# Optimization experiments

Hardware: AMD Instinct MI355X
Metric: run time of the kernel (lower is better)

## Reference

```python
import jax, jax.numpy as jnp
import numpy as np

N, C, A, CI = 32768, 512, 64, 1024  # n_locations, content_size, address_size, controller_input_size
EPS = 1e-7


def setup_inputs() -> dict:
    key = jax.random.key(0)
    ks = jax.random.split(key, 12)
    g = lambda i, shape, s=1.0: jax.random.normal(ks[i], shape, dtype=jnp.float32) * s
    xav = lambda i, shape: g(i, shape, float(np.sqrt(2.0 / (shape[0] + shape[1]))))
    return {
        "controller_hidden_state": g(0, (N, 1)),
        "controller_input": g(1, (CI, 1)),
        "memory_contents": g(2, (N, C), 0.5),
        "memory_addresses": xav(3, (N, A)),
        "exp_mov_avg_similarity": g(4, (N, 1), 0.1),
        "W_query": xav(5, (C + A, N)),
        "b_query": jnp.zeros((C + A, 1), jnp.float32),
        "u_sharpen": xav(6, (1, N)),
        "b_sharpen": jnp.zeros((1,), jnp.float32),
        "u_lru": xav(7, (1, N)),
        "b_lru": jnp.zeros((1,), jnp.float32),
        "W_erase": xav(8, (C, N)),
        "b_erase": jnp.zeros((C, 1), jnp.float32),
        "W_content_hidden": xav(9, (C, N)),
        "W_content_input": xav(10, (C, CI)),
        "u_content_alpha": xav(11, (N + CI, 1)),
        "b_content_alpha": jnp.zeros((1, 1), jnp.float32),
    }


def reference(controller_hidden_state, controller_input, memory_contents, memory_addresses,
              exp_mov_avg_similarity, W_query, b_query, u_sharpen, b_sharpen, u_lru, b_lru,
              W_erase, b_erase, W_content_hidden, W_content_input, u_content_alpha,
              b_content_alpha):
    h, x = controller_hidden_state, controller_input
    # ---- address_memory ----
    full_mem = jnp.concatenate([memory_addresses, memory_contents], axis=1)  # [N, A+C]
    query = W_query @ h + b_query                                            # [A+C, 1]
    beta = jax.nn.softplus(u_sharpen @ h + b_sharpen) + 1.0                  # [1, 1]
    q = query[:, 0]
    q_norm = jnp.maximum(jnp.linalg.norm(q), EPS)
    m_norm = jnp.maximum(jnp.linalg.norm(full_mem, axis=1), EPS)             # [N]
    cos = (full_mem @ q) / (m_norm * q_norm)                                 # [N] cosine sim per location
    sim = (beta[0, 0] * cos)[:, None]                                        # [N, 1]
    gamma = jax.nn.sigmoid(u_lru @ h + b_lru)                                # [1, 1] LRU gate
    addr = jax.nn.softmax(sim - gamma * exp_mov_avg_similarity, axis=0)      # [N, 1]
    # (state buffer update, next-step only): new_ema = 0.1*ema + 0.9*sim
    # ---- update (vectorized erase/write over all N locations) ----
    erase = W_erase @ h + b_erase                                            # [C, 1]
    alpha = u_content_alpha.T @ jnp.concatenate([h, x], axis=0) + b_content_alpha  # [1, 1]
    cand = jax.nn.relu(W_content_hidden @ h + alpha * (W_content_input @ x))       # [C, 1]
    new_mem = (1.0 - addr * erase.T) * memory_contents + addr * cand.T       # [N, C]
    # ---- read (on updated memory) ----
    new_full = jnp.concatenate([memory_addresses, new_mem], axis=1)          # [N, A+C]
    read = new_full.T @ addr                                                 # [A+C, 1]
    return read
```

## Files before the change

### kernel.cpp

```cpp
#include <hip/hip_runtime.h>
#include <hip/hip_bf16.h>
#include <math.h>

#define NN 32768
#define CC 512
#define AA 64
#define CIN 1024
#define EPSV 1e-7f


#define QOFF 2128
#define STOFF 2704
#define SCOFF 4240
#define PAOFF 5264
#define PMOFF 38032

typedef float floatx4 __attribute__((ext_vector_type(4)));

__device__ __forceinline__ float4 ntload4(const float4* p) {
    floatx4 v = __builtin_nontemporal_load(reinterpret_cast<const floatx4*>(p));
    return make_float4(v.x, v.y, v.z, v.w);
}
__device__ __forceinline__ float ntloadf(const float* p) {
    return __builtin_nontemporal_load(p);
}

__global__ __launch_bounds__(256) void k1_gemv(
    const float* __restrict__ h, const float* __restrict__ x,
    const float* __restrict__ Wq, const float* __restrict__ Wer,
    const float* __restrict__ Wch, const float* __restrict__ Wci,
    const float* __restrict__ ush, const float* __restrict__ ulr,
    const float* __restrict__ uca, float* __restrict__ ws)
{
    const int b = blockIdx.x, tid = threadIdx.x;
    const int wave = tid >> 6, lane = tid & 63;
    __shared__ float hs[4096];
    __shared__ float red[4][8];

    if (b < 1600) {
        const int rg = b >> 3, chunk = b & 7;
        const float4* h4 = reinterpret_cast<const float4*>(h) + chunk * 1024;
        float4* hs4 = reinterpret_cast<float4*>(hs);
        #pragma unroll
        for (int k = 0; k < 4; ++k) hs4[k * 256 + tid] = h4[k * 256 + tid];
        __syncthreads();
        const int r0 = rg * 8;
        const float* mat; int base;
        if (r0 < 576)       { mat = Wq;  base = 0; }
        else if (r0 < 1088) { mat = Wer; base = 576; }
        else                { mat = Wch; base = 1088; }
        const float4* m4 = reinterpret_cast<const float4*>(
            mat + (size_t)(r0 - base) * NN + chunk * 4096);
        const int rs = NN / 4;
        float acc[8] = {0,0,0,0,0,0,0,0};
        float4 cur[8];
        #pragma unroll
        for (int r = 0; r < 8; ++r) cur[r] = ntload4(m4 + (size_t)r * rs + tid);
        #pragma unroll
        for (int it = 0; it < 4; ++it) {
            float4 nxt[8];
            if (it < 3) {
                #pragma unroll
                for (int r = 0; r < 8; ++r)
                    nxt[r] = ntload4(m4 + (size_t)r * rs + (it + 1) * 256 + tid);
            }
            float4 hb = hs4[it * 256 + tid];
            #pragma unroll
            for (int r = 0; r < 8; ++r)
                acc[r] += cur[r].x * hb.x + cur[r].y * hb.y +
                          cur[r].z * hb.z + cur[r].w * hb.w;
            if (it < 3) {
                #pragma unroll
                for (int r = 0; r < 8; ++r) cur[r] = nxt[r];
            }
        }
        #pragma unroll
        for (int r = 0; r < 8; ++r) {
            #pragma unroll
            for (int off = 32; off >= 1; off >>= 1)
                acc[r] += __shfl_xor(acc[r], off);
        }
        if (lane == 0) {
            #pragma unroll
            for (int r = 0; r < 8; ++r) red[wave][r] = acc[r];
        }
        __syncthreads();
        if (tid < 8) {
            float v = red[0][tid] + red[1][tid] + red[2][tid] + red[3][tid];
            atomicAdd(ws + r0 + tid, v);
        }
    } else if (b < 1664) {
        const int rg = b - 1600;
        float4 xv = reinterpret_cast<const float4*>(x)[tid];
        const float4* m4 = reinterpret_cast<const float4*>(
            Wci + (size_t)rg * 8 * CIN);
        float acc[8];
        #pragma unroll
        for (int r = 0; r < 8; ++r) {
            float4 a = ntload4(m4 + r * 256 + tid);
            acc[r] = a.x * xv.x + a.y * xv.y + a.z * xv.z + a.w * xv.w;
        }
        #pragma unroll
        for (int r = 0; r < 8; ++r) {
            #pragma unroll
            for (int off = 32; off >= 1; off >>= 1)
                acc[r] += __shfl_xor(acc[r], off);
        }
        if (lane == 0) {
            #pragma unroll
            for (int r = 0; r < 8; ++r) red[wave][r] = acc[r];
        }
        __syncthreads();
        if (tid < 8) {
            float v = red[0][tid] + red[1][tid] + red[2][tid] + red[3][tid];
            ws[1600 + rg * 8 + tid] = v;
        }
    } else {
        const int t = b - 1664, sd = t >> 3, chunk = t & 7;
        const float* vec = (sd == 0) ? ush : (sd == 1) ? ulr : uca;
        const float4* v4 = reinterpret_cast<const float4*>(vec) + chunk * 1024;
        const float4* h4 = reinterpret_cast<const float4*>(h) + chunk * 1024;
        float acc = 0.f;
        #pragma unroll
        for (int it = 0; it < 4; ++it) {
            float4 a = v4[it * 256 + tid];
            float4 hb = h4[it * 256 + tid];
            acc += a.x * hb.x + a.y * hb.y + a.z * hb.z + a.w * hb.w;
        }
        if (sd == 2 && chunk == 0) {
            float4 a = reinterpret_cast<const float4*>(uca)[NN / 4 + tid];
            float4 xv = reinterpret_cast<const float4*>(x)[tid];
            acc += a.x * xv.x + a.y * xv.y + a.z * xv.z + a.w * xv.w;
        }
        #pragma unroll
        for (int off = 32; off >= 1; off >>= 1)
            acc += __shfl_xor(acc, off);
        if (lane == 0) red[wave][0] = acc;
        __syncthreads();
        if (tid == 0)
            atomicAdd(ws + 2112 + sd,
                      red[0][0] + red[1][0] + red[2][0] + red[3][0]);
    }
}

__global__ __launch_bounds__(256) void k1b_scalars(
    const float* __restrict__ bq, const float* __restrict__ bsh,
    const float* __restrict__ blr, const float* __restrict__ bca,
    float* __restrict__ ws)
{
    __shared__ float red[256];
    const int tid = threadIdx.x;
    float s = 0.f;
    for (int j = tid; j < 576; j += 256) {
        float q = ws[j] + bq[j];
        ws[QOFF + j] = q;
        s += q * q;
    }
    red[tid] = s; __syncthreads();
    for (int st = 128; st > 0; st >>= 1) {
        if (tid < st) red[tid] += red[tid + st];
        __syncthreads();
    }
    if (tid == 0) {
        float qn = fmaxf(sqrtf(red[0]), EPSV);
        float bp = ws[2112] + bsh[0];
        float beta = (bp > 20.f ? bp : log1pf(expf(bp))) + 1.0f;
        float gp = ws[2113] + blr[0];
        float gamma = 1.f / (1.f + expf(-gp));
        float alpha = ws[2114] + bca[0];
        ws[2112] = beta; ws[2113] = gamma; ws[2114] = alpha; ws[2115] = qn;
    }
}

__global__ __launch_bounds__(512) void k2f_fused(
    const float* __restrict__ Mm, const float* __restrict__ Ad,
    const float* __restrict__ ema, const float* __restrict__ ws,
    float* __restrict__ pm, float* __restrict__ pa, float* __restrict__ stats)
{
    __shared__ float lw[8][1092];
    const int b = blockIdx.x, tid = threadIdx.x, wave = tid >> 6, lane = tid & 63;
    const float beta = ws[2112], gamma = ws[2113], qn = ws[2115];
    const float ql = ws[QOFF + lane];
    float4 qa = *reinterpret_cast<const float4*>(ws + QOFF + 64 + lane * 8);
    float4 qb = *reinterpret_cast<const float4*>(ws + QOFF + 68 + lane * 8);
    float qm[8] = {qa.x, qa.y, qa.z, qa.w, qb.x, qb.y, qb.z, qb.w};

    float a1[8] = {0,0,0,0,0,0,0,0};
    float a2[8] = {0,0,0,0,0,0,0,0};
    float aA = 0.f, m_run = -1e30f, Z = 0.f, S2 = 0.f;
    const int base = b * 64 + wave * 8;
    for (int j = 0; j < 8; ++j) {
        const int i = base + j;
        float a = ntloadf(Ad + (size_t)i * AA + lane);
        float4 m0 = ntload4(reinterpret_cast<const float4*>(Mm + (size_t)i * CC + lane * 8));
        float4 m1 = ntload4(reinterpret_cast<const float4*>(Mm + (size_t)i * CC + lane * 8 + 4));
        float mm[8] = {m0.x, m0.y, m0.z, m0.w, m1.x, m1.y, m1.z, m1.w};
        float dot = a * ql, nn = a * a;
        #pragma unroll
        for (int k = 0; k < 8; ++k) { float f = mm[k]; dot += f * qm[k]; nn += f * f; }
        #pragma unroll
        for (int off = 32; off >= 1; off >>= 1) {
            dot += __shfl_xor(dot, off);
            nn  += __shfl_xor(nn, off);
        }
        float mn = fmaxf(sqrtf(nn), EPSV);
        float s = beta * (dot / (mn * qn)) - gamma * ema[i];
        if (s > m_run) {
            float f = expf(m_run - s);
            float f2 = f * f;
            Z *= f; S2 *= f2; aA *= f;
            #pragma unroll
            for (int k = 0; k < 8; ++k) { a1[k] *= f; a2[k] *= f2; }
            m_run = s;
        }
        float w = expf(s - m_run);
        float w2 = w * w;
        Z += w; S2 += w2; aA += w * a;
        #pragma unroll
        for (int k = 0; k < 8; ++k) { a1[k] += w * mm[k]; a2[k] += w2 * mm[k]; }
    }
    #pragma unroll
    for (int k = 0; k < 8; ++k) {
        lw[wave][lane * 8 + k] = a1[k];
        lw[wave][512 + lane * 8 + k] = a2[k];
    }
    lw[wave][1024 + lane] = aA;
    if (lane == 0) { lw[wave][1088] = m_run; lw[wave][1089] = Z; lw[wave][1090] = S2; }
    __syncthreads();
    float mb = lw[0][1088];
    #pragma unroll
    for (int w = 1; w < 8; ++w) mb = fmaxf(mb, lw[w][1088]);
    float fw[8];
    #pragma unroll
    for (int w = 0; w < 8; ++w) fw[w] = expf(lw[w][1088] - mb);
    for (int e = tid; e < 1024; e += 512) {
        float v = 0.f;
        if (e < 512) {
            #pragma unroll
            for (int w = 0; w < 8; ++w) v += fw[w] * lw[w][e];
        } else {
            #pragma unroll
            for (int w = 0; w < 8; ++w) v += fw[w] * fw[w] * lw[w][e];
        }
        pm[(size_t)e * 512 + b] = v;
    }
    if (tid < 64) {
        float v = 0.f;
        #pragma unroll
        for (int w = 0; w < 8; ++w) v += fw[w] * lw[w][1024 + tid];
        pa[tid * 512 + b] = v;
    }
    if (tid == 0) {
        float Zl = 0.f, S2l = 0.f;
        #pragma unroll
        for (int w = 0; w < 8; ++w) {
            Zl  += fw[w] * lw[w][1089];
            S2l += fw[w] * fw[w] * lw[w][1090];
        }
        stats[b] = mb; stats[512 + b] = Zl; stats[1024 + b] = S2l;
    }
}

__global__ __launch_bounds__(512) void k3g(
    const float* __restrict__ stats, float* __restrict__ sc,
    float* __restrict__ ws)
{
    __shared__ float red[512];
    const int t = threadIdx.x;
    float m = stats[t];
    red[t] = m; __syncthreads();
    for (int st = 256; st > 0; st >>= 1) {
        if (t < st) red[t] = fmaxf(red[t], red[t + st]);
        __syncthreads();
    }
    float mx = red[0]; __syncthreads();
    float e1 = expf(m - mx);
    red[t] = e1 * stats[512 + t]; __syncthreads();
    for (int st = 256; st > 0; st >>= 1) {
        if (t < st) red[t] += red[t + st];
        __syncthreads();
    }
    float Zg = red[0]; __syncthreads();
    red[t] = e1 * e1 * stats[1024 + t]; __syncthreads();
    for (int st = 256; st > 0; st >>= 1) {
        if (t < st) red[t] += red[t + st];
        __syncthreads();
    }
    float S2s = red[0];
    float iZ = 1.f / Zg;
    sc[t] = e1 * iZ;
    sc[512 + t] = e1 * e1 * iZ * iZ;
    if (t == 0) ws[2118] = S2s * iZ * iZ;
}

__global__ __launch_bounds__(256) void k5_final(
    const float* __restrict__ ws, const float* __restrict__ pm,
    const float* __restrict__ pa, const float* __restrict__ sc,
    const float* __restrict__ ber, float* __restrict__ out)
{
    __shared__ float red[256];
    const int b = blockIdx.x, tid = threadIdx.x;
    if (b < 64) {
        float v = sc[tid] * pa[b * 512 + tid] + sc[tid + 256] * pa[b * 512 + tid + 256];
        red[tid] = v; __syncthreads();
        for (int st = 128; st > 0; st >>= 1) {
            if (tid < st) red[tid] += red[tid + st];
            __syncthreads();
        }
        if (tid == 0) out[b] = red[0];
    } else {
        const int c = b - 64;
        float v1 = sc[tid] * pm[(size_t)c * 512 + tid]
                 + sc[tid + 256] * pm[(size_t)c * 512 + tid + 256];
        float v2 = sc[512 + tid] * pm[(size_t)(512 + c) * 512 + tid]
                 + sc[512 + tid + 256] * pm[(size_t)(512 + c) * 512 + tid + 256];
        red[tid] = v1; __syncthreads();
        for (int st = 128; st > 0; st >>= 1) {
            if (tid < st) red[tid] += red[tid + st];
            __syncthreads();
        }
        float s1 = red[0];
        __syncthreads();
        red[tid] = v2; __syncthreads();
        for (int st = 128; st > 0; st >>= 1) {
            if (tid < st) red[tid] += red[tid + st];
            __syncthreads();
        }
        if (tid == 0) {
            float s2v = red[0];
            float er = ws[576 + c] + ber[c];
            float ch = ws[1088 + c], cx = ws[1600 + c];
            float alpha = ws[2114], S2 = ws[2118];
            float cand = fmaxf(ch + alpha * cx, 0.f);
            out[64 + c] = s1 - er * s2v + S2 * cand;
        }
    }
}

extern "C" void kernel_launch(void* const* d_in, const int* in_sizes, int n_in,
                              void* d_out, int out_size, void* d_ws, size_t ws_size,
                              hipStream_t stream)
{
    const float* h   = (const float*)d_in[0];
    const float* x   = (const float*)d_in[1];
    const float* Mm  = (const float*)d_in[2];
    const float* Ad  = (const float*)d_in[3];
    const float* ema = (const float*)d_in[4];
    const float* Wq  = (const float*)d_in[5];
    const float* bq  = (const float*)d_in[6];
    const float* ush = (const float*)d_in[7];
    const float* bsh = (const float*)d_in[8];
    const float* ulr = (const float*)d_in[9];
    const float* blr = (const float*)d_in[10];
    const float* Wer = (const float*)d_in[11];
    const float* ber = (const float*)d_in[12];
    const float* Wch = (const float*)d_in[13];
    const float* Wci = (const float*)d_in[14];
    const float* uca = (const float*)d_in[15];
    const float* bca = (const float*)d_in[16];

    float* ws    = (float*)d_ws;
    float* stats = ws + STOFF;
    float* sc    = ws + SCOFF;
    float* pa    = ws + PAOFF;
    float* pm    = ws + PMOFF;
    float* out   = (float*)d_out;

    (void)hipMemsetAsync(ws, 0, QOFF * sizeof(float), stream);

    hipLaunchKernelGGL(k1_gemv,     dim3(1688), dim3(256), 0, stream,
                       h, x, Wq, Wer, Wch, Wci, ush, ulr, uca, ws);
    hipLaunchKernelGGL(k1b_scalars, dim3(1),    dim3(256), 0, stream,
                       bq, bsh, blr, bca, ws);
    hipLaunchKernelGGL(k2f_fused,   dim3(512),  dim3(512), 0, stream,
                       Mm, Ad, ema, ws, pm, pa, stats);
    hipLaunchKernelGGL(k3g,         dim3(1),    dim3(512), 0, stream, stats, sc, ws);
    hipLaunchKernelGGL(k5_final,    dim3(576),  dim3(256), 0, stream,
                       ws, pm, pa, sc, ber, out);
}
```

Measured before the change: 281.0 us.

## Restructure pipeline: query GEMV first, overlap erase/content GEMVs with memory pass

The query GEMV now runs alone in a first kernel. The erase, content and alpha GEMVs are merged into the same launch as the memory cosine/softmax pass, so the two groups of bandwidth-bound work can overlap, and each memory block recomputes the query norm and scalars itself. Atomics and the memset are replaced by per-chunk partial sums that consumers add up. The separate scalar and global-stats kernels are folded into the final kernel, which reduces the launch count from five to three. The cost is redundant per-block recomputation of the query vector and global stats, plus a larger grid with mixed block roles.

Result: no change. 283.5 us (+0.9%).

```diff
diff --git a/kernel.cpp b/kernel.cpp
--- a/kernel.cpp
+++ b/kernel.cpp
@@ -9,11 +9,11 @@
 #define EPSV 1e-7f
 
 
-#define QOFF 2128
-#define STOFF 2704
-#define SCOFF 4240
-#define PAOFF 5264
-#define PMOFF 38032
+#define PDS   1604
+#define CXOFF 12832
+#define STOFF 13344
+#define PAOFF 14880
+#define PMOFF 47648
 
 typedef float floatx4 __attribute__((ext_vector_type(4)));
 
@@ -25,19 +25,17 @@
     return __builtin_nontemporal_load(p);
 }
 
-__global__ __launch_bounds__(256) void k1_gemv(
-    const float* __restrict__ h, const float* __restrict__ x,
-    const float* __restrict__ Wq, const float* __restrict__ Wer,
-    const float* __restrict__ Wch, const float* __restrict__ Wci,
+__global__ __launch_bounds__(256) void k1q(
+    const float* __restrict__ h, const float* __restrict__ Wq,
     const float* __restrict__ ush, const float* __restrict__ ulr,
-    const float* __restrict__ uca, float* __restrict__ ws)
+    float* __restrict__ ws)
 {
+    __shared__ float hs[4096];
+    __shared__ float red[4][8];
     const int b = blockIdx.x, tid = threadIdx.x;
     const int wave = tid >> 6, lane = tid & 63;
-    __shared__ float hs[4096];
-    __shared__ float red[4][8];
-
-    if (b < 1600) {
+
+    if (b < 576) {
         const int rg = b >> 3, chunk = b & 7;
         const float4* h4 = reinterpret_cast<const float4*>(h) + chunk * 1024;
         float4* hs4 = reinterpret_cast<float4*>(hs);
@@ -45,12 +43,8 @@
         for (int k = 0; k < 4; ++k) hs4[k * 256 + tid] = h4[k * 256 + tid];
         __syncthreads();
         const int r0 = rg * 8;
-        const float* mat; int base;
-        if (r0 < 576)       { mat = Wq;  base = 0; }
-        else if (r0 < 1088) { mat = Wer; base = 576; }
-        else                { mat = Wch; base = 1088; }
         const float4* m4 = reinterpret_cast<const float4*>(
-            mat + (size_t)(r0 - base) * NN + chunk * 4096);
+            Wq + (size_t)r0 * NN + chunk * 4096);
         const int rs = NN / 4;
         float acc[8] = {0,0,0,0,0,0,0,0};
         float4 cur[8];
@@ -87,37 +81,11 @@
         __syncthreads();
         if (tid < 8) {
             float v = red[0][tid] + red[1][tid] + red[2][tid] + red[3][tid];
-            atomicAdd(ws + r0 + tid, v);
-        }
-    } else if (b < 1664) {
-        const int rg = b - 1600;
-        float4 xv = reinterpret_cast<const float4*>(x)[tid];
-        const float4* m4 = reinterpret_cast<const float4*>(
-            Wci + (size_t)rg * 8 * CIN);
-        float acc[8];
-        #pragma unroll
-        for (int r = 0; r < 8; ++r) {
-            float4 a = ntload4(m4 + r * 256 + tid);
-            acc[r] = a.x * xv.x + a.y * xv.y + a.z * xv.z + a.w * xv.w;
-        }
-        #pragma unroll
-        for (int r = 0; r < 8; ++r) {
-            #pragma unroll
-            for (int off = 32; off >= 1; off >>= 1)
-                acc[r] += __shfl_xor(acc[r], off);
-        }
-        if (lane == 0) {
-            #pragma unroll
-            for (int r = 0; r < 8; ++r) red[wave][r] = acc[r];
-        }
-        __syncthreads();
-        if (tid < 8) {
-            float v = red[0][tid] + red[1][tid] + red[2][tid] + red[3][tid];
-            ws[1600 + rg * 8 + tid] = v;
+            ws[chunk * PDS + r0 + tid] = v;
         }
     } else {
-        const int t = b - 1664, sd = t >> 3, chunk = t & 7;
-        const float* vec = (sd == 0) ? ush : (sd == 1) ? ulr : uca;
+        const int t = b - 576, sd = t >> 3, chunk = t & 7;
+        const float* vec = sd ? ulr : ush;
         const float4* v4 = reinterpret_cast<const float4*>(vec) + chunk * 1024;
         const float4* h4 = reinterpret_cast<const float4*>(h) + chunk * 1024;
         float acc = 0.f;
@@ -127,199 +95,274 @@
             float4 hb = h4[it * 256 + tid];
             acc += a.x * hb.x + a.y * hb.y + a.z * hb.z + a.w * hb.w;
         }
-        if (sd == 2 && chunk == 0) {
+        #pragma unroll
+        for (int off = 32; off >= 1; off >>= 1)
+            acc += __shfl_xor(acc, off);
+        if (lane == 0) red[wave][0] = acc;
+        __syncthreads();
+        if (tid == 0)
+            ws[chunk * PDS + 1600 + sd] =
+                red[0][0] + red[1][0] + red[2][0] + red[3][0];
+    }
+}
+
+__global__ __launch_bounds__(512) void k2big(
+    const float* __restrict__ h, const float* __restrict__ x,
+    const float* __restrict__ Wer, const float* __restrict__ Wch,
+    const float* __restrict__ Wci, const float* __restrict__ uca,
+    const float* __restrict__ Mm, const float* __restrict__ Ad,
+    const float* __restrict__ ema,
+    const float* __restrict__ bq, const float* __restrict__ bsh,
+    const float* __restrict__ blr,
+    float* __restrict__ ws)
+{
+    __shared__ float smem[8736];
+    const int g = blockIdx.x, tid = threadIdx.x;
+    const int wave = tid >> 6, lane = tid & 63;
+    float* contx = ws + CXOFF;
+    float* stats = ws + STOFF;
+    float* pa = ws + PAOFF;
+    float* pm = ws + PMOFF;
+
+    if (g < 1024) {
+        const int rg = g >> 3, chunk = g & 7;
+        const int r = 576 + rg * 8 + wave;
+        const float4* h4 = reinterpret_cast<const float4*>(h) + chunk * 1024;
+        float4* hs4 = reinterpret_cast<float4*>(smem);
+        hs4[tid] = h4[tid];
+        hs4[tid + 512] = h4[tid + 512];
+        __syncthreads();
+        const float* mat = (r < 1088) ? Wer : Wch;
+        const int base = (r < 1088) ? 576 : 1088;
+        const float4* m4 = reinterpret_cast<const float4*>(
+            mat + (size_t)(r - base) * NN + chunk * 4096);
+        float acc = 0.f;
+        #pragma unroll
+        for (int it = 0; it < 16; ++it) {
+            float4 a = ntload4(m4 + it * 64 + lane);
+            float4 hb = hs4[it * 64 + lane];
+            acc += a.x * hb.x + a.y * hb.y + a.z * hb.z + a.w * hb.w;
+        }
+        #pragma unroll
+        for (int off = 32; off >= 1; off >>= 1)
+            acc += __shfl_xor(acc, off);
+        if (lane == 0) ws[chunk * PDS + r] = acc;
+    } else if (g < 1088) {
+        const int wg = g - 1024;
+        const int r = wg * 8 + wave;
+        float4* hs4 = reinterpret_cast<float4*>(smem);
+        if (tid < 256) hs4[tid] = reinterpret_cast<const float4*>(x)[tid];
+        __syncthreads();
+        const float4* m4 = reinterpret_cast<const float4*>(Wci + (size_t)r * CIN);
+        float acc = 0.f;
+        #pragma unroll
+        for (int it = 0; it < 4; ++it) {
+            float4 a = ntload4(m4 + it * 64 + lane);
+            float4 hb = hs4[it * 64 + lane];
+            acc += a.x * hb.x + a.y * hb.y + a.z * hb.z + a.w * hb.w;
+        }
+        #pragma unroll
+        for (int off = 32; off >= 1; off >>= 1)
+            acc += __shfl_xor(acc, off);
+        if (lane == 0) contx[r] = acc;
+    } else if (g < 1096) {
+        const int chunk = g - 1088;
+        const float4* u4 = reinterpret_cast<const float4*>(uca) + chunk * 1024;
+        const float4* h4 = reinterpret_cast<const float4*>(h) + chunk * 1024;
+        float acc = 0.f;
+        {
+            float4 a = u4[tid], hb = h4[tid];
+            acc += a.x * hb.x + a.y * hb.y + a.z * hb.z + a.w * hb.w;
+            a = u4[tid + 512]; hb = h4[tid + 512];
+            acc += a.x * hb.x + a.y * hb.y + a.z * hb.z + a.w * hb.w;
+        }
+        if (chunk == 0 && tid < 256) {
             float4 a = reinterpret_cast<const float4*>(uca)[NN / 4 + tid];
             float4 xv = reinterpret_cast<const float4*>(x)[tid];
             acc += a.x * xv.x + a.y * xv.y + a.z * xv.z + a.w * xv.w;
         }
-        #pragma unroll
-        for (int off = 32; off >= 1; off >>= 1)
-            acc += __shfl_xor(acc, off);
-        if (lane == 0) red[wave][0] = acc;
-        __syncthreads();
-        if (tid == 0)
-            atomicAdd(ws + 2112 + sd,
-                      red[0][0] + red[1][0] + red[2][0] + red[3][0]);
-    }
-}
-
-__global__ __launch_bounds__(256) void k1b_scalars(
-    const float* __restrict__ bq, const float* __restrict__ bsh,
-    const float* __restrict__ blr, const float* __restrict__ bca,
-    float* __restrict__ ws)
+        smem[tid] = acc; __syncthreads();
+        for (int st = 256; st > 0; st >>= 1) {
+            if (tid < st) smem[tid] += smem[tid + st];
+            __syncthreads();
+        }
+        if (tid == 0) ws[chunk * PDS + 1602] = smem[0];
+    } else {
+        const int b = g - 1096;
+        float* qs  = smem;
+        float* red = smem + 576;
+        float* scl = smem + 1088;
+        float sq = 0.f;
+        for (int j = tid; j < 576; j += 512) {
+            float q = bq[j];
+            #pragma unroll
+            for (int ch = 0; ch < 8; ++ch) q += ws[ch * PDS + j];
+            qs[j] = q; sq += q * q;
+        }
+        red[tid] = sq; __syncthreads();
+        for (int st = 256; st > 0; st >>= 1) {
+            if (tid < st) red[tid] += red[tid + st];
+            __syncthreads();
+        }
+        if (tid == 0) {
+            scl[0] = fmaxf(sqrtf(red[0]), EPSV);
+            float sb = bsh[0], sl = blr[0];
+            #pragma unroll
+            for (int ch = 0; ch < 8; ++ch) {
+                sb += ws[ch * PDS + 1600];
+                sl += ws[ch * PDS + 1601];
+            }
+            scl[1] = (sb > 20.f ? sb : log1pf(expf(sb))) + 1.0f;
+            scl[2] = 1.f / (1.f + expf(-sl));
+        }
+        __syncthreads();
+        const float qn = scl[0], beta = scl[1], gamma = scl[2];
+        const float ql = qs[lane];
+        float4 qa = *reinterpret_cast<const float4*>(qs + 64 + lane * 8);
+        float4 qb2 = *reinterpret_cast<const float4*>(qs + 68 + lane * 8);
+        float qm[8] = {qa.x, qa.y, qa.z, qa.w, qb2.x, qb2.y, qb2.z, qb2.w};
+        __syncthreads();
+
+        float a1[8] = {0,0,0,0,0,0,0,0};
+        float a2[8] = {0,0,0,0,0,0,0,0};
+        float aA = 0.f, m_run = -1e30f, Z = 0.f, S2 = 0.f;
+        const int base = b * 64 + wave * 8;
+        for (int j = 0; j < 8; ++j) {
+            const int i = base + j;
+            float a = ntloadf(Ad + (size_t)i * AA + lane);
+            float4 m0 = ntload4(reinterpret_cast<const float4*>(Mm + (size_t)i * CC + lane * 8));
+            float4 m1 = ntload4(reinterpret_cast<const float4*>(Mm + (size_t)i * CC + lane * 8 + 4));
+            float mm[8] = {m0.x, m0.y, m0.z, m0.w, m1.x, m1.y, m1.z, m1.w};
+            float dot = a * ql, nn = a * a;
+            #pragma unroll
+            for (int k = 0; k < 8; ++k) { float f = mm[k]; dot += f * qm[k]; nn += f * f; }
+            #pragma unroll
+            for (int off = 32; off >= 1; off >>= 1) {
+                dot += __shfl_xor(dot, off);
+                nn  += __shfl_xor(nn, off);
+            }
+            float mn = fmaxf(sqrtf(nn), EPSV);
+            float s = beta * (dot / (mn * qn)) - gamma * ema[i];
+            if (s > m_run) {
+                float f = expf(m_run - s);
+                float f2 = f * f;
+                Z *= f; S2 *= f2; aA *= f;
+                #pragma unroll
+                for (int k = 0; k < 8; ++k) { a1[k] *= f; a2[k] *= f2; }
+                m_run = s;
+            }
+            float w = expf(s - m_run);
+            float w2 = w * w;
+            Z += w; S2 += w2; aA += w * a;
+            #pragma unroll
+            for (int k = 0; k < 8; ++k) { a1[k] += w * mm[k]; a2[k] += w2 * mm[k]; }
+        }
+        float* lw = smem;
+        float* mylw = lw + wave * 1092;
+        #pragma unroll
+        for (int k = 0; k < 8; ++k) {
+            mylw[lane * 8 + k] = a1[k];
+            mylw[512 + lane * 8 + k] = a2[k];
+        }
+        mylw[1024 + lane] = aA;
+        if (lane == 0) { mylw[1088] = m_run; mylw[1089] = Z; mylw[1090] = S2; }
+        __syncthreads();
+        float mb = lw[1088];
+        #pragma unroll
+        for (int w = 1; w < 8; ++w) mb = fmaxf(mb, lw[w * 1092 + 1088]);
+        float fw[8];
+        #pragma unroll
+        for (int w = 0; w < 8; ++w) fw[w] = expf(lw[w * 1092 + 1088] - mb);
+        for (int e = tid; e < 1024; e += 512) {
+            float v = 0.f;
+            if (e < 512) {
+                #pragma unroll
+                for (int w = 0; w < 8; ++w) v += fw[w] * lw[w * 1092 + e];
+            } else {
+                #pragma unroll
+                for (int w = 0; w < 8; ++w) v += fw[w] * fw[w] * lw[w * 1092 + e];
+            }
+            pm[(size_t)e * 512 + b] = v;
+        }
+        if (tid < 64) {
+            float v = 0.f;
+            #pragma unroll
+            for (int w = 0; w < 8; ++w) v += fw[w] * lw[w * 1092 + 1024 + tid];
+            pa[tid * 512 + b] = v;
+        }
+        if (tid == 0) {
+            float Zl = 0.f, S2l = 0.f;
+            #pragma unroll
+            for (int w = 0; w < 8; ++w) {
+                Zl  += fw[w] * lw[w * 1092 + 1089];
+                S2l += fw[w] * fw[w] * lw[w * 1092 + 1090];
+            }
+            stats[b] = mb; stats[512 + b] = Zl; stats[1024 + b] = S2l;
+        }
+    }
+}
+
+__global__ __launch_bounds__(256) void k5_final(
+    const float* __restrict__ ws, const float* __restrict__ ber,
+    const float* __restrict__ bca, float* __restrict__ out)
 {
     __shared__ float red[256];
-    const int tid = threadIdx.x;
-    float s = 0.f;
-    for (int j = tid; j < 576; j += 256) {
-        float q = ws[j] + bq[j];
-        ws[QOFF + j] = q;
-        s += q * q;
-    }
-    red[tid] = s; __syncthreads();
+    __shared__ float bc[2];
+    const int b = blockIdx.x, tid = threadIdx.x;
+    const float* stats = ws + STOFF;
+    const float* pa = ws + PAOFF;
+    const float* pm = ws + PMOFF;
+    const float* contx = ws + CXOFF;
+
+    float m = fmaxf(stats[tid], stats[tid + 256]);
+    red[tid] = m; __syncthreads();
+    for (int st = 128; st > 0; st >>= 1) {
+        if (tid < st) red[tid] = fmaxf(red[tid], red[tid + st]);
+        __syncthreads();
+    }
+    if (tid == 0) bc[0] = red[0];
+    __syncthreads();
+    const float mx = bc[0];
+    const float e1a = expf(stats[tid] - mx);
+    const float e1b = expf(stats[tid + 256] - mx);
+    red[tid] = e1a * stats[512 + tid] + e1b * stats[512 + tid + 256];
+    __syncthreads();
     for (int st = 128; st > 0; st >>= 1) {
         if (tid < st) red[tid] += red[tid + st];
         __syncthreads();
     }
-    if (tid == 0) {
-        float qn = fmaxf(sqrtf(red[0]), EPSV);
-        float bp = ws[2112] + bsh[0];
-        float beta = (bp > 20.f ? bp : log1pf(expf(bp))) + 1.0f;
-        float gp = ws[2113] + blr[0];
-        float gamma = 1.f / (1.f + expf(-gp));
-        float alpha = ws[2114] + bca[0];
-        ws[2112] = beta; ws[2113] = gamma; ws[2114] = alpha; ws[2115] = qn;
-    }
-}
-
-__global__ __launch_bounds__(512) void k2f_fused(
-    const float* __restrict__ Mm, const float* __restrict__ Ad,
-    const float* __restrict__ ema, const float* __restrict__ ws,
-    float* __restrict__ pm, float* __restrict__ pa, float* __restrict__ stats)
-{
-    __shared__ float lw[8][1092];
-    const int b = blockIdx.x, tid = threadIdx.x, wave = tid >> 6, lane = tid & 63;
-    const float beta = ws[2112], gamma = ws[2113], qn = ws[2115];
-    const float ql = ws[QOFF + lane];
-    float4 qa = *reinterpret_cast<const float4*>(ws + QOFF + 64 + lane * 8);
-    float4 qb = *reinterpret_cast<const float4*>(ws + QOFF + 68 + lane * 8);
-    float qm[8] = {qa.x, qa.y, qa.z, qa.w, qb.x, qb.y, qb.z, qb.w};
-
-    float a1[8] = {0,0,0,0,0,0,0,0};
-    float a2[8] = {0,0,0,0,0,0,0,0};
-    float aA = 0.f, m_run = -1e30f, Z = 0.f, S2 = 0.f;
-    const int base = b * 64 + wave * 8;
-    for (int j = 0; j < 8; ++j) {
-        const int i = base + j;
-        float a = ntloadf(Ad + (size_t)i * AA + lane);
-        float4 m0 = ntload4(reinterpret_cast<const float4*>(Mm + (size_t)i * CC + lane * 8));
-        float4 m1 = ntload4(reinterpret_cast<const float4*>(Mm + (size_t)i * CC + lane * 8 + 4));
-        float mm[8] = {m0.x, m0.y, m0.z, m0.w, m1.x, m1.y, m1.z, m1.w};
-        float dot = a * ql, nn = a * a;
-        #pragma unroll
-        for (int k = 0; k < 8; ++k) { float f = mm[k]; dot += f * qm[k]; nn += f * f; }
-        #pragma unroll
-        for (int off = 32; off >= 1; off >>= 1) {
-            dot += __shfl_xor(dot, off);
-            nn  += __shfl_xor(nn, off);
-        }
-        float mn = fmaxf(sqrtf(nn), EPSV);
-        float s = beta * (dot / (mn * qn)) - gamma * ema[i];
-        if (s > m_run) {
-            float f = expf(m_run - s);
-            float f2 = f * f;
-            Z *= f; S2 *= f2; aA *= f;
-            #pragma unroll
-            for (int k = 0; k < 8; ++k) { a1[k] *= f; a2[k] *= f2; }
-            m_run = s;
-        }
-        float w = expf(s - m_run);
-        float w2 = w * w;
-        Z += w; S2 += w2; aA += w * a;
-        #pragma unroll
-        for (int k = 0; k < 8; ++k) { a1[k] += w * mm[k]; a2[k] += w2 * mm[k]; }
-    }
-    #pragma unroll
-    for (int k = 0; k < 8; ++k) {
-        lw[wave][lane * 8 + k] = a1[k];
-        lw[wave][512 + lane * 8 + k] = a2[k];
-    }
-    lw[wave][1024 + lane] = aA;
-    if (lane == 0) { lw[wave][1088] = m_run; lw[wave][1089] = Z; lw[wave][1090] = S2; }
+    const float Zg = red[0];
     __syncthreads();
-    float mb = lw[0][1088];
-    #pragma unroll
-    for (int w = 1; w < 8; ++w) mb = fmaxf(mb, lw[w][1088]);
-    float fw[8];
-    #pragma unroll
-    for (int w = 0; w < 8; ++w) fw[w] = expf(lw[w][1088] - mb);
-    for (int e = tid; e < 1024; e += 512) {
-        float v = 0.f;
-        if (e < 512) {
-            #pragma unroll
-            for (int w = 0; w < 8; ++w) v += fw[w] * lw[w][e];
-        } else {
-            #pragma unroll
-            for (int w = 0; w < 8; ++w) v += fw[w] * fw[w] * lw[w][e];
-        }
-        pm[(size_t)e * 512 + b] = v;
-    }
-    if (tid < 64) {
-        float v = 0.f;
-        #pragma unroll
-        for (int w = 0; w < 8; ++w) v += fw[w] * lw[w][1024 + tid];
-        pa[tid * 512 + b] = v;
-    }
-    if (tid == 0) {
-        float Zl = 0.f, S2l = 0.f;
-        #pragma unroll
-        for (int w = 0; w < 8; ++w) {
-            Zl  += fw[w] * lw[w][1089];
-            S2l += fw[w] * fw[w] * lw[w][1090];
-        }
-        stats[b] = mb; stats[512 + b] = Zl; stats[1024 + b] = S2l;
-    }
-}
-
-__global__ __launch_bounds__(512) void k3g(
-    const float* __restrict__ stats, float* __restrict__ sc,
-    float* __restrict__ ws)
-{
-    __shared__ float red[512];
-    const int t = threadIdx.x;
-    float m = stats[t];
-    red[t] = m; __syncthreads();
-    for (int st = 256; st > 0; st >>= 1) {
-        if (t < st) red[t] = fmaxf(red[t], red[t + st]);
-        __syncthreads();
-    }
-    float mx = red[0]; __syncthreads();
-    float e1 = expf(m - mx);
-    red[t] = e1 * stats[512 + t]; __syncthreads();
-    for (int st = 256; st > 0; st >>= 1) {
-        if (t < st) red[t] += red[t + st];
-        __syncthreads();
-    }
-    float Zg = red[0]; __syncthreads();
-    red[t] = e1 * e1 * stats[1024 + t]; __syncthreads();
-    for (int st = 256; st > 0; st >>= 1) {
-        if (t < st) red[t] += red[t + st];
-        __syncthreads();
-    }
-    float S2s = red[0];
-    float iZ = 1.f / Zg;
-    sc[t] = e1 * iZ;
-    sc[512 + t] = e1 * e1 * iZ * iZ;
-    if (t == 0) ws[2118] = S2s * iZ * iZ;
-}
-
-__global__ __launch_bounds__(256) void k5_final(
-    const float* __restrict__ ws, const float* __restrict__ pm,
-    const float* __restrict__ pa, const float* __restrict__ sc,
-    const float* __restrict__ ber, float* __restrict__ out)
-{
-    __shared__ float red[256];
-    const int b = blockIdx.x, tid = threadIdx.x;
+    red[tid] = e1a * e1a * stats[1024 + tid] + e1b * e1b * stats[1024 + tid + 256];
+    __syncthreads();
+    for (int st = 128; st > 0; st >>= 1) {
+        if (tid < st) red[tid] += red[tid + st];
+        __syncthreads();
+    }
+    const float iZ = 1.f / Zg;
+    const float S2g = red[0] * iZ * iZ;
+    __syncthreads();
+
     if (b < 64) {
-        float v = sc[tid] * pa[b * 512 + tid] + sc[tid + 256] * pa[b * 512 + tid + 256];
-        red[tid] = v; __syncthreads();
+        red[tid] = e1a * pa[b * 512 + tid] + e1b * pa[b * 512 + tid + 256];
+        __syncthreads();
         for (int st = 128; st > 0; st >>= 1) {
             if (tid < st) red[tid] += red[tid + st];
             __syncthreads();
         }
-        if (tid == 0) out[b] = red[0];
+        if (tid == 0) out[b] = iZ * red[0];
     } else {
         const int c = b - 64;
-        float v1 = sc[tid] * pm[(size_t)c * 512 + tid]
-                 + sc[tid + 256] * pm[(size_t)c * 512 + tid + 256];
-        float v2 = sc[512 + tid] * pm[(size_t)(512 + c) * 512 + tid]
-                 + sc[512 + tid + 256] * pm[(size_t)(512 + c) * 512 + tid + 256];
+        float v1 = e1a * pm[(size_t)c * 512 + tid]
+                 + e1b * pm[(size_t)c * 512 + tid + 256];
+        float v2 = e1a * e1a * pm[(size_t)(512 + c) * 512 + tid]
+                 + e1b * e1b * pm[(size_t)(512 + c) * 512 + tid + 256];
         red[tid] = v1; __syncthreads();
         for (int st = 128; st > 0; st >>= 1) {
             if (tid < st) red[tid] += red[tid + st];
             __syncthreads();
         }
-        float s1 = red[0];
+        const float s1 = iZ * red[0];
         __syncthreads();
         red[tid] = v2; __syncthreads();
         for (int st = 128; st > 0; st >>= 1) {
@@ -327,12 +370,16 @@
             __syncthreads();
         }
         if (tid == 0) {
-            float s2v = red[0];
-            float er = ws[576 + c] + ber[c];
-            float ch = ws[1088 + c], cx = ws[1600 + c];
-            float alpha = ws[2114], S2 = ws[2118];
-            float cand = fmaxf(ch + alpha * cx, 0.f);
-            out[64 + c] = s1 - er * s2v + S2 * cand;
+            const float s2v = iZ * iZ * red[0];
+            float er = ber[c], chv = 0.f, alpha = bca[0];
+            #pragma unroll
+            for (int ch = 0; ch < 8; ++ch) {
+                er    += ws[ch * PDS + 576 + c];
+                chv   += ws[ch * PDS + 1088 + c];
+                alpha += ws[ch * PDS + 1602];
+            }
+            const float cand = fmaxf(chv + alpha * contx[c], 0.f);
+            out[64 + c] = s1 - er * s2v + S2g * cand;
         }
     }
 }
@@ -359,22 +406,13 @@
     const float* uca = (const float*)d_in[15];
     const float* bca = (const float*)d_in[16];
 
-    float* ws    = (float*)d_ws;
-    float* stats = ws + STOFF;
-    float* sc    = ws + SCOFF;
-    float* pa    = ws + PAOFF;
-    float* pm    = ws + PMOFF;
-    float* out   = (float*)d_out;
-
-    (void)hipMemsetAsync(ws, 0, QOFF * sizeof(float), stream);
-
-    hipLaunchKernelGGL(k1_gemv,     dim3(1688), dim3(256), 0, stream,
-                       h, x, Wq, Wer, Wch, Wci, ush, ulr, uca, ws);
-    hipLaunchKernelGGL(k1b_scalars, dim3(1),    dim3(256), 0, stream,
-                       bq, bsh, blr, bca, ws);
-    hipLaunchKernelGGL(k2f_fused,   dim3(512),  dim3(512), 0, stream,
-                       Mm, Ad, ema, ws, pm, pa, stats);
-    hipLaunchKernelGGL(k3g,         dim3(1),    dim3(512), 0, stream, stats, sc, ws);
-    hipLaunchKernelGGL(k5_final,    dim3(576),  dim3(256), 0, stream,
-                       ws, pm, pa, sc, ber, out);
-}
+    float* ws  = (float*)d_ws;
+    float* out = (float*)d_out;
+
+    hipLaunchKernelGGL(k1q,     dim3(592),  dim3(256), 0, stream,
+                       h, Wq, ush, ulr, ws);
+    hipLaunchKernelGGL(k2big,   dim3(1608), dim3(512), 0, stream,
+                       h, x, Wer, Wch, Wci, uca, Mm, Ad, ema, bq, bsh, blr, ws);
+    hipLaunchKernelGGL(k5_final, dim3(576), dim3(256), 0, stream,
+                       ws, ber, bca, out);
+}
```
